# Kernel optimization log

Measured on AMD Instinct MI355X. Metric: run time of the kernel, lower is better.

The kernel has to match this reference:

```python
import jax, jax.numpy as jnp
import numpy as np

EPS = 1e-5


def _lerp_t(y, out_t):
    # trilinear interpolate with align_corners=True where only the T axis changes size
    T = y.shape[2]
    pos = jnp.arange(out_t) * ((T - 1) / (out_t - 1))
    i0 = jnp.floor(pos).astype(jnp.int32)
    i1 = jnp.minimum(i0 + 1, T - 1)
    w = (pos - i0).astype(y.dtype)[None, None, :, None, None]
    return jnp.take(y, i0, axis=2) * (1 - w) + jnp.take(y, i1, axis=2) * w


def setup_inputs() -> dict:
    key = jax.random.key(0)
    ks = jax.random.split(key, 8)
    B, C, T, H, W = 2, 32, 64, 64, 64
    N = 512
    Cf = 32   # projection_nin (backbone feature channels)
    Ch = Cf // 2
    x = jax.random.normal(ks[0], (B, C, T, H, W), jnp.float32)
    coord = jax.random.randint(ks[1], (B, N, 2), 0, H)
    # backbone stand-in: two pointwise 1x1x1 conv heads
    Wf = jax.random.normal(ks[2], (Cf, C), jnp.float32) * 0.05
    bf = jnp.zeros((Cf,), jnp.float32)
    Wr = jax.random.normal(ks[3], (1, C), jnp.float32) * 0.05
    br = jnp.zeros((1,), jnp.float32)
    # projection1: Conv1d(Cf->Ch,k=1) + BN1d(Ch) + ReLU + Conv1d(Ch->Ch,k=1)
    W1 = jax.random.normal(ks[4], (Ch, Cf), jnp.float32) * 0.1
    b1 = jnp.zeros((Ch,), jnp.float32)
    gamma = jnp.ones((Ch,), jnp.float32)
    beta = jnp.zeros((Ch,), jnp.float32)
    W2 = jax.random.normal(ks[5], (Ch, Ch), jnp.float32) * 0.1
    b2 = jnp.zeros((Ch,), jnp.float32)
    return {"x": x, "coord": coord, "Wf": Wf, "bf": bf, "Wr": Wr, "br": br,
            "W1": W1, "b1": b1, "gamma": gamma, "beta": beta, "W2": W2, "b2": b2,
            "orgt": 400, "featT": 400}


def reference(x, coord, Wf, bf, Wr, br, W1, b1, gamma, beta, W2, b2, orgt, featT):
    B, C, T, H, W = x.shape
    # backbone (pointwise conv3d heads)
    feat = jnp.einsum('oc,bcthw->bothw', Wf, x) + bf[None, :, None, None, None]
    result = jnp.einsum('oc,bcthw->bothw', Wr, x) + br[None, :, None, None, None]
    # trilinear resize along T only (H,W unchanged, align_corners=True -> identity)
    feat = _lerp_t(feat, featT)        # [B,Cf,featT,H,W]
    result = _lerp_t(result, orgt)     # [B,1,orgt,H,W]
    # presample: per-sample spatial gather at coord (h,w) pairs
    Cf = feat.shape[1]
    idx = coord[..., 0] * W + coord[..., 1]                      # [B,N]
    flat = feat.reshape(B, Cf, featT, H * W)
    g = jnp.take_along_axis(flat, idx[:, None, None, :], axis=3)  # [B,Cf,featT,N]
    g = g.reshape(B, Cf, -1)                                      # [B,Cf,featT*N]
    # projection1: pointwise conv -> BN (training stats) -> ReLU -> pointwise conv
    h = jnp.einsum('oc,bcl->bol', W1, g) + b1[None, :, None]
    mu = h.mean(axis=(0, 2), keepdims=True)
    var = ((h - mu) ** 2).mean(axis=(0, 2), keepdims=True)
    h = (h - mu) * jax.lax.rsqrt(var + EPS) * gamma[None, :, None] + beta[None, :, None]
    h = jax.nn.relu(h)
    out = jnp.einsum('oc,bcl->bol', W2, h) + b2[None, :, None]
    return out, result
```

## Files before the change

kernel.cpp:

```cpp
#include <hip/hip_runtime.h>
#include <stdint.h>

#define BB   2
#define CC   32
#define TT   64
#define HWH  4096
#define NN   512
#define CFF  32
#define CHH  16
#define TOUT 400
#define LL   (TOUT*NN)

__device__ __forceinline__ void lerp_coeff(int to, int& i0, int& i1, float& w){
  const float step = (float)(63.0 / 399.0);
  float pos = (float)to * step;
  i0 = (int)floorf(pos);
  if (i0 > TT - 1) i0 = TT - 1;
  i1 = i0 + 1; if (i1 > TT - 1) i1 = TT - 1;
  w = pos - (float)i0;
}

__global__ __launch_bounds__(256) void k_r(const float* __restrict__ x, const float* __restrict__ Wr,
                                           const float* __restrict__ br, float* __restrict__ r,
                                           float* __restrict__ stats){
  if (blockIdx.x == 0 && threadIdx.x < 32) stats[threadIdx.x] = 0.f;
  int tid = blockIdx.x * 256 + threadIdx.x;
  int hw0 = (tid & 1023) << 2;
  int t   = (tid >> 10) & 63;
  int b   = tid >> 16;
  float br0 = br[0];
  float4 acc = make_float4(br0, br0, br0, br0);
  const float* xp = x + ((size_t)(b * CC) * TT + t) * HWH + hw0;
  #pragma unroll
  for (int c = 0; c < CC; ++c){
    float4 v = *reinterpret_cast<const float4*>(xp + (size_t)c * TT * HWH);
    float w = Wr[c];
    acc.x += w * v.x;  acc.y += w * v.y;  acc.z += w * v.z;  acc.w += w * v.w;
  }
  *reinterpret_cast<float4*>(r + ((size_t)(b * TT + t)) * HWH + hw0) = acc;
}

__global__ __launch_bounds__(256) void k_result(const float* __restrict__ r, float* __restrict__ outR){
  int tid = blockIdx.x * 256 + threadIdx.x;
  int hw0  = (tid & 1023) << 2;
  int rest = tid >> 10;
  int b  = rest >= TOUT ? 1 : 0;
  int to = rest - b * TOUT;
  int i0, i1; float w;
  lerp_coeff(to, i0, i1, w);
  float4 a = *reinterpret_cast<const float4*>(r + ((size_t)(b * TT + i0)) * HWH + hw0);
  float4 c = *reinterpret_cast<const float4*>(r + ((size_t)(b * TT + i1)) * HWH + hw0);
  float4 o;
  o.x = a.x + w * (c.x - a.x);
  o.y = a.y + w * (c.y - a.y);
  o.z = a.z + w * (c.z - a.z);
  o.w = a.w + w * (c.w - a.w);
  *reinterpret_cast<float4*>(outR + ((size_t)(b * TOUT + to)) * HWH + hw0) = o;
}

__global__ __launch_bounds__(256) void k_z(const float* __restrict__ x, const int* __restrict__ coord,
                                           const float* __restrict__ Wf, const float* __restrict__ bfv,
                                           const float* __restrict__ W1, const float* __restrict__ b1,
                                           float* __restrict__ Z){
  __shared__ float sWT[CC][CHH];
  __shared__ float scz[CHH];
  for (int i = threadIdx.x; i < CHH * CC; i += 256){
    int o = i >> 5, c = i & 31;
    float v = 0.f;
    #pragma unroll
    for (int k = 0; k < CFF; ++k) v += W1[o * CFF + k] * Wf[k * CC + c];
    sWT[c][o] = v;
  }
  if (threadIdx.x < CHH){
    float v = b1[threadIdx.x];
    #pragma unroll
    for (int k = 0; k < CFF; ++k) v += W1[threadIdx.x * CFF + k] * bfv[k];
    scz[threadIdx.x] = v;
  }
  __syncthreads();
  int lane = threadIdx.x & 63;
  int sub  = threadIdx.x & 3;
  int e = blockIdx.x * 64 + ((int)threadIdx.x >> 2);
  int n = e & 511, t = (e >> 9) & 63, b = e >> 15;
  int h  = coord[(b * NN + n) * 2 + 0];
  int wq = coord[(b * NN + n) * 2 + 1];
  int hw = h * 64 + wq;
  const float* xp = x + (((size_t)(b * CC + sub * 8)) * TT + t) * HWH + hw;
  float xv[8];
  #pragma unroll
  for (int j = 0; j < 8; ++j) xv[j] = xp[(size_t)j * (TT * HWH)];
  float acc0 = scz[sub * 4], acc1 = scz[sub * 4 + 1], acc2 = scz[sub * 4 + 2], acc3 = scz[sub * 4 + 3];
  int grp = lane & ~3;
  #pragma unroll
  for (int j = 0; j < 8; ++j){
    #pragma unroll
    for (int src = 0; src < 4; ++src){
      float xc = __shfl(xv[j], grp + src, 64);
      int c = src * 8 + j;
      const float4 w4 = *reinterpret_cast<const float4*>(&sWT[c][sub * 4]);
      acc0 += w4.x * xc;  acc1 += w4.y * xc;  acc2 += w4.z * xc;  acc3 += w4.w * xc;
    }
  }
  *reinterpret_cast<float4*>(Z + ((size_t)((b * TT + t) * NN + n)) * CHH + sub * 4)
      = make_float4(acc0, acc1, acc2, acc3);
}

__global__ __launch_bounds__(256) void k_mom(const float* __restrict__ Z, float* __restrict__ stats){
  __shared__ float sco[192];
  __shared__ float red[4][32];
  if (threadIdx.x < 192) sco[threadIdx.x] = 0.f;
  __syncthreads();
  for (int to = threadIdx.x; to < TOUT; to += 256){
    int i0, i1; float w;
    lerp_coeff(to, i0, i1, w);
    if (i1 == i0){
      atomicAdd(&sco[i0], 1.f);  atomicAdd(&sco[64 + i0], 1.f);
    } else {
      float u = 1.f - w;
      atomicAdd(&sco[i0], u);        atomicAdd(&sco[64 + i0], u * u);
      atomicAdd(&sco[i1], w);        atomicAdd(&sco[64 + i1], w * w);
      atomicAdd(&sco[128 + i0], 2.f * w * u);
    }
  }
  __syncthreads();
  int t = threadIdx.x & 63;
  int e = blockIdx.x * 4 + ((int)threadIdx.x >> 6);
  int b = e >> 9, n = e & 511;
  const float* zp = Z + ((size_t)((b * TT + t) * NN + n)) * CHH;
  float z[CHH];
  #pragma unroll
  for (int c = 0; c < CHH; c += 4){
    float4 v = *reinterpret_cast<const float4*>(zp + c);
    z[c] = v.x; z[c+1] = v.y; z[c+2] = v.z; z[c+3] = v.w;
  }
  float qt = sco[t], at = sco[64 + t], ct = sco[128 + t];
  float v1[CHH], v2[CHH];
  #pragma unroll
  for (int o = 0; o < CHH; ++o){
    float zn = __shfl_down(z[o], 1, 64);
    v1[o] = qt * z[o];
    v2[o] = at * z[o] * z[o] + ct * z[o] * zn;
  }
  #pragma unroll
  for (int o = 0; o < CHH; ++o){
    #pragma unroll
    for (int s = 32; s > 0; s >>= 1){
      v1[o] += __shfl_down(v1[o], s, 64);
      v2[o] += __shfl_down(v2[o], s, 64);
    }
  }
  int wave = threadIdx.x >> 6, lane = threadIdx.x & 63;
  if (lane == 0){
    #pragma unroll
    for (int o = 0; o < CHH; ++o){ red[wave][o] = v1[o]; red[wave][16 + o] = v2[o]; }
  }
  __syncthreads();
  if (threadIdx.x < 32){
    float v = red[0][threadIdx.x] + red[1][threadIdx.x] + red[2][threadIdx.x] + red[3][threadIdx.x];
    atomicAdd(stats + threadIdx.x, v);
  }
}

__global__ __launch_bounds__(256) void k_out(const float* __restrict__ Z, const float* __restrict__ W2,
                                             const float* __restrict__ b2, const float* __restrict__ gamma,
                                             const float* __restrict__ beta, const float* __restrict__ stats,
                                             float* __restrict__ out){
  __shared__ float sW2[CHH][CHH];
  __shared__ float sb2[CHH], ssc[CHH], ssh[CHH];
  for (int i = threadIdx.x; i < CHH * CHH; i += 256) sW2[i >> 4][i & 15] = W2[i];
  if (threadIdx.x < CHH){
    int o = threadIdx.x;
    const float inv = 1.0f / (float)(BB * (long long)LL);
    float mu  = stats[o] * inv;
    float var = stats[16 + o] * inv - mu * mu;
    float sc  = gamma[o] * (1.0f / sqrtf(var + 1e-5f));
    ssc[o] = sc;
    ssh[o] = beta[o] - mu * sc;
    sb2[o] = b2[o];
  }
  __syncthreads();
  int xcd = blockIdx.x & 7, loc = blockIdx.x >> 3;
  int eb = xcd * 200 + loc;
  int li  = eb * 256 + (int)threadIdx.x;
  int b   = li / LL;
  int rem = li - b * LL;
  int to  = rem >> 9;
  int n   = rem & 511;
  int i0, i1; float w;
  lerp_coeff(to, i0, i1, w);
  const float* z0 = Z + ((size_t)((b * TT + i0) * NN + n)) * CHH;
  const float* z1 = Z + ((size_t)((b * TT + i1) * NN + n)) * CHH;
  float hr[CHH];
  #pragma unroll
  for (int c = 0; c < CHH; c += 4){
    float4 a = *reinterpret_cast<const float4*>(z0 + c);
    float4 d = *reinterpret_cast<const float4*>(z1 + c);
    float h0 = a.x + w * (d.x - a.x);
    float h1 = a.y + w * (d.y - a.y);
    float h2 = a.z + w * (d.z - a.z);
    float h3 = a.w + w * (d.w - a.w);
    hr[c]   = fmaxf(h0 * ssc[c]   + ssh[c],   0.0f);
    hr[c+1] = fmaxf(h1 * ssc[c+1] + ssh[c+1], 0.0f);
    hr[c+2] = fmaxf(h2 * ssc[c+2] + ssh[c+2], 0.0f);
    hr[c+3] = fmaxf(h3 * ssc[c+3] + ssh[c+3], 0.0f);
  }
  #pragma unroll
  for (int o2 = 0; o2 < CHH; ++o2){
    float v = sb2[o2];
    #pragma unroll
    for (int o = 0; o < CHH; ++o) v += sW2[o2][o] * hr[o];
    out[((size_t)(b * CHH + o2)) * LL + rem] = v;
  }
}

extern "C" void kernel_launch(void* const* d_in, const int* in_sizes, int n_in,
                              void* d_out, int out_size, void* d_ws, size_t ws_size,
                              hipStream_t stream){
  (void)in_sizes; (void)n_in; (void)out_size; (void)ws_size;
  const float* x     = (const float*)d_in[0];
  const int*   coord = (const int*)d_in[1];
  const float* Wf    = (const float*)d_in[2];
  const float* bfv   = (const float*)d_in[3];
  const float* Wr    = (const float*)d_in[4];
  const float* br    = (const float*)d_in[5];
  const float* W1    = (const float*)d_in[6];
  const float* b1    = (const float*)d_in[7];
  const float* gamma = (const float*)d_in[8];
  const float* beta  = (const float*)d_in[9];
  const float* W2    = (const float*)d_in[10];
  const float* b2    = (const float*)d_in[11];

  float* ws    = (float*)d_ws;
  float* r     = ws;
  float* Z     = ws + 524288;
  float* stats = ws + 524288 + 1048576;

  float* out  = (float*)d_out;
  float* outR = out + (size_t)BB * CHH * LL;

  k_r     <<<512,  256, 0, stream>>>(x, Wr, br, r, stats);
  k_z     <<<1024, 256, 0, stream>>>(x, coord, Wf, bfv, W1, b1, Z);
  k_result<<<3200, 256, 0, stream>>>(r, outR);
  k_mom   <<<256,  256, 0, stream>>>(Z, stats);
  k_out   <<<1600, 256, 0, stream>>>(Z, W2, b2, gamma, beta, stats, out);
}
```

Before: 179.5 us.

## Fuse sampled-column projection into result-head kernel via shared-memory column capture

Merges the gather-and-project kernel into the pointwise result-head kernel. Each block covers one (b,t) and a quarter of the HW plane, builds a shared-memory hash list of the sampled coordinates that fall in that quarter, captures those x columns while streaming x for the result head, then computes Z from shared memory and scatters it to every duplicate sample index. This removes the second pass of strided global loads over x and one kernel launch. In exchange it uses a large shared-memory footprint (about 72 KB), which limits occupancy of the bandwidth-bound head kernel, and adds atomics and extra synchronization.

```diff
diff --git a/kernel.cpp b/kernel.cpp
--- a/kernel.cpp
+++ b/kernel.cpp
@@ -21,13 +21,57 @@
 }
 
 __global__ __launch_bounds__(256) void k_r(const float* __restrict__ x, const float* __restrict__ Wr,
-                                           const float* __restrict__ br, float* __restrict__ r,
+                                           const float* __restrict__ br, const int* __restrict__ coord,
+                                           const float* __restrict__ Wf, const float* __restrict__ bfv,
+                                           const float* __restrict__ W1, const float* __restrict__ b1,
+                                           float* __restrict__ r, float* __restrict__ Z,
                                            float* __restrict__ stats){
+  __shared__ float sCol[512 * 33];
+  __shared__ int   sHead[1024];
+  __shared__ int   sNext[512];
+  __shared__ int   sColHw[512];
+  __shared__ float sWT[CC][CHH];
+  __shared__ float sbz[CHH];
+  __shared__ int   sCnt;
+
+  int q = blockIdx.x & 3, t = (blockIdx.x >> 2) & 63, b = (int)blockIdx.x >> 8;
   if (blockIdx.x == 0 && threadIdx.x < 32) stats[threadIdx.x] = 0.f;
-  int tid = blockIdx.x * 256 + threadIdx.x;
-  int hw0 = (tid & 1023) << 2;
-  int t   = (tid >> 10) & 63;
-  int b   = tid >> 16;
+
+  for (int i = threadIdx.x; i < CHH * CC; i += 256){
+    int o = i >> 5, c = i & 31;
+    float v = 0.f;
+    #pragma unroll
+    for (int k = 0; k < CFF; ++k) v += W1[o * CFF + k] * Wf[k * CC + c];
+    sWT[c][o] = v;
+  }
+  if (threadIdx.x < CHH){
+    float v = b1[threadIdx.x];
+    #pragma unroll
+    for (int k = 0; k < CFF; ++k) v += W1[threadIdx.x * CFF + k] * bfv[k];
+    sbz[threadIdx.x] = v;
+  }
+  #pragma unroll
+  for (int j = 0; j < 4; ++j) sHead[threadIdx.x * 4 + j] = -1;
+  if (threadIdx.x == 0) sCnt = 0;
+  __syncthreads();
+  #pragma unroll
+  for (int k = 0; k < 2; ++k){
+    int n  = (int)threadIdx.x + 256 * k;
+    int hh = coord[(b * NN + n) * 2], ww = coord[(b * NN + n) * 2 + 1];
+    int hw = hh * 64 + ww;
+    if ((hw >> 10) == q) sNext[n] = atomicExch(&sHead[hw & 1023], n);
+  }
+  __syncthreads();
+  int lhw0 = (int)threadIdx.x * 4;
+  int slot[4];
+  #pragma unroll
+  for (int j = 0; j < 4; ++j){
+    bool m = (sHead[lhw0 + j] != -1);
+    slot[j] = m ? atomicAdd(&sCnt, 1) : -1;
+    if (m) sColHw[slot[j]] = lhw0 + j;
+  }
+
+  int hw0 = q * 1024 + lhw0;
   float br0 = br[0];
   float4 acc = make_float4(br0, br0, br0, br0);
   const float* xp = x + ((size_t)(b * CC) * TT + t) * HWH + hw0;
@@ -36,8 +80,43 @@
     float4 v = *reinterpret_cast<const float4*>(xp + (size_t)c * TT * HWH);
     float w = Wr[c];
     acc.x += w * v.x;  acc.y += w * v.y;  acc.z += w * v.z;  acc.w += w * v.w;
+    if (slot[0] >= 0) sCol[slot[0] * 33 + c] = v.x;
+    if (slot[1] >= 0) sCol[slot[1] * 33 + c] = v.y;
+    if (slot[2] >= 0) sCol[slot[2] * 33 + c] = v.z;
+    if (slot[3] >= 0) sCol[slot[3] * 33 + c] = v.w;
   }
   *reinterpret_cast<float4*>(r + ((size_t)(b * TT + t)) * HWH + hw0) = acc;
+
+  __syncthreads();
+  int ncols = sCnt;
+  for (int k2 = threadIdx.x; k2 < ncols; k2 += 256){
+    float z[CHH];
+    #pragma unroll
+    for (int o = 0; o < CHH; ++o) z[o] = sbz[o];
+    #pragma unroll
+    for (int c = 0; c < CC; ++c){
+      float xc = sCol[k2 * 33 + c];
+      #pragma unroll
+      for (int o4 = 0; o4 < CHH; o4 += 4){
+        const float4 w4 = *reinterpret_cast<const float4*>(&sWT[c][o4]);
+        z[o4]   += w4.x * xc;  z[o4+1] += w4.y * xc;
+        z[o4+2] += w4.z * xc;  z[o4+3] += w4.w * xc;
+      }
+    }
+    float4 z0 = make_float4(z[0],  z[1],  z[2],  z[3]);
+    float4 z1 = make_float4(z[4],  z[5],  z[6],  z[7]);
+    float4 z2 = make_float4(z[8],  z[9],  z[10], z[11]);
+    float4 z3 = make_float4(z[12], z[13], z[14], z[15]);
+    int n = sHead[sColHw[k2]];
+    while (n != -1){
+      float* zp = Z + ((size_t)((b * TT + t) * NN + n)) * CHH;
+      *reinterpret_cast<float4*>(zp)      = z0;
+      *reinterpret_cast<float4*>(zp + 4)  = z1;
+      *reinterpret_cast<float4*>(zp + 8)  = z2;
+      *reinterpret_cast<float4*>(zp + 12) = z3;
+      n = sNext[n];
+    }
+  }
 }
 
 __global__ __launch_bounds__(256) void k_result(const float* __restrict__ r, float* __restrict__ outR){
@@ -58,53 +137,6 @@
   *reinterpret_cast<float4*>(outR + ((size_t)(b * TOUT + to)) * HWH + hw0) = o;
 }
 
-__global__ __launch_bounds__(256) void k_z(const float* __restrict__ x, const int* __restrict__ coord,
-                                           const float* __restrict__ Wf, const float* __restrict__ bfv,
-                                           const float* __restrict__ W1, const float* __restrict__ b1,
-                                           float* __restrict__ Z){
-  __shared__ float sWT[CC][CHH];
-  __shared__ float scz[CHH];
-  for (int i = threadIdx.x; i < CHH * CC; i += 256){
-    int o = i >> 5, c = i & 31;
-    float v = 0.f;
-    #pragma unroll
-    for (int k = 0; k < CFF; ++k) v += W1[o * CFF + k] * Wf[k * CC + c];
-    sWT[c][o] = v;
-  }
-  if (threadIdx.x < CHH){
-    float v = b1[threadIdx.x];
-    #pragma unroll
-    for (int k = 0; k < CFF; ++k) v += W1[threadIdx.x * CFF + k] * bfv[k];
-    scz[threadIdx.x] = v;
-  }
-  __syncthreads();
-  int lane = threadIdx.x & 63;
-  int sub  = threadIdx.x & 3;
-  int e = blockIdx.x * 64 + ((int)threadIdx.x >> 2);
-  int n = e & 511, t = (e >> 9) & 63, b = e >> 15;
-  int h  = coord[(b * NN + n) * 2 + 0];
-  int wq = coord[(b * NN + n) * 2 + 1];
-  int hw = h * 64 + wq;
-  const float* xp = x + (((size_t)(b * CC + sub * 8)) * TT + t) * HWH + hw;
-  float xv[8];
-  #pragma unroll
-  for (int j = 0; j < 8; ++j) xv[j] = xp[(size_t)j * (TT * HWH)];
-  float acc0 = scz[sub * 4], acc1 = scz[sub * 4 + 1], acc2 = scz[sub * 4 + 2], acc3 = scz[sub * 4 + 3];
-  int grp = lane & ~3;
-  #pragma unroll
-  for (int j = 0; j < 8; ++j){
-    #pragma unroll
-    for (int src = 0; src < 4; ++src){
-      float xc = __shfl(xv[j], grp + src, 64);
-      int c = src * 8 + j;
-      const float4 w4 = *reinterpret_cast<const float4*>(&sWT[c][sub * 4]);
-      acc0 += w4.x * xc;  acc1 += w4.y * xc;  acc2 += w4.z * xc;  acc3 += w4.w * xc;
-    }
-  }
-  *reinterpret_cast<float4*>(Z + ((size_t)((b * TT + t) * NN + n)) * CHH + sub * 4)
-      = make_float4(acc0, acc1, acc2, acc3);
-}
-
 __global__ __launch_bounds__(256) void k_mom(const float* __restrict__ Z, float* __restrict__ stats){
   __shared__ float sco[192];
   __shared__ float red[4][32];
@@ -238,8 +270,7 @@
   float* out  = (float*)d_out;
   float* outR = out + (size_t)BB * CHH * LL;
 
-  k_r     <<<512,  256, 0, stream>>>(x, Wr, br, r, stats);
-  k_z     <<<1024, 256, 0, stream>>>(x, coord, Wf, bfv, W1, b1, Z);
+  k_r     <<<512,  256, 0, stream>>>(x, Wr, br, coord, Wf, bfv, W1, b1, r, Z, stats);
   k_result<<<3200, 256, 0, stream>>>(r, outR);
   k_mom   <<<256,  256, 0, stream>>>(Z, stats);
   k_out   <<<1600, 256, 0, stream>>>(Z, W2, b2, gamma, beta, stats, out);
```

Measured after the change: 190.8 us. 1.06x slower.
